# Kernel optimization log

Hardware: AMD Instinct MI355X
Metric: run time of the kernel (lower is better)

## Reference

```python
import jax, jax.numpy as jnp
import numpy as np

WIDTH = 256          # hidden width of FiLM MLP
NUM_FREQ = 8         # NeRF frequencies
BASE_FREQ = 1.25
TWO_PI = 2.0 * np.pi


def _uniform_linear(k, out_dim, in_dim):
    # torch nn.Linear default init: U(-1/sqrt(in), 1/sqrt(in))
    kw, kb = jax.random.split(k)
    s = 1.0 / np.sqrt(in_dim)
    W = jax.random.uniform(kw, (out_dim, in_dim), minval=-s, maxval=s, dtype=jnp.float32)
    b = jax.random.uniform(kb, (out_dim,), minval=-s, maxval=s, dtype=jnp.float32)
    return W, b


def setup_inputs() -> dict:
    key = jax.random.key(0)
    ks = jax.random.split(key, 14)
    B, T = 1024, 512
    latent_dim, lstm_hidden_dim = 128, 128
    spatial_dim, dir_dim, num_directions = 32, 8, 6
    emb_out = 2 * NUM_FREQ + 1                      # 17 (include_input)
    mod_in = latent_dim + lstm_hidden_dim + spatial_dim + dir_dim  # 296
    num_mods = 2 * WIDTH                            # width*(depth-1) = 512

    W_mod, b_mod = _uniform_linear(ks[0], num_mods, mod_in)
    W0, b0 = _uniform_linear(ks[1], WIDTH, emb_out)
    W1, b1 = _uniform_linear(ks[2], WIDTH, WIDTH)
    Wo, bo = _uniform_linear(ks[3], 1, WIDTH)
    Bmat = jax.random.normal(ks[4], (2, 16), dtype=jnp.float32) * 0.1  # sigma=0.1
    Ws1, bs1 = _uniform_linear(ks[5], 64, 32)
    Ws2, bs2 = _uniform_linear(ks[6], spatial_dim, 64)
    dir_emb = jax.random.normal(ks[7], (num_directions, dir_dim), dtype=jnp.float32)

    return dict(
        coords=jax.random.uniform(ks[8], (B, T, 1), dtype=jnp.float32),
        code=jax.random.normal(ks[9], (B, latent_dim), dtype=jnp.float32),
        hs=jax.random.normal(ks[10], (B, T, lstm_hidden_dim), dtype=jnp.float32),
        x_statics=jax.random.normal(ks[11], (B, 2), dtype=jnp.float32),
        dir_idx=jax.random.randint(ks[12], (1024,), 0, num_directions, dtype=jnp.int32),
        W_mod=W_mod, b_mod=b_mod, W0=W0, b0=b0, W1=W1, b1=b1, Wo=Wo, bo=bo,
        Bmat=Bmat, Ws1=Ws1, bs1=bs1, Ws2=Ws2, bs2=bs2, dir_emb=dir_emb,
    )


def reference(coords, code, hs, x_statics, dir_idx,
              W_mod, b_mod, W0, b0, W1, b1, Wo, bo,
              Bmat, Ws1, bs1, Ws2, bs2, dir_emb):
    B, T, _ = coords.shape

    # --- NeRF encoding: (B,T,1) -> (B,T,17) ---
    bands = BASE_FREQ * jnp.arange(0, NUM_FREQ, dtype=coords.dtype)     # (8,)
    winded = (coords[..., None, :] * bands[None, None, :, None]).reshape(B, T, -1)
    pos = jnp.concatenate([coords, jnp.sin(winded), jnp.cos(winded)], axis=-1)

    # --- Static encoder: latlon Fourier MLP + direction embedding ---
    proj = TWO_PI * (x_statics @ Bmat)                                  # (B,16)
    feats = jnp.concatenate([jnp.sin(proj), jnp.cos(proj)], axis=-1)    # (B,32)
    h = jax.nn.gelu(feats @ Ws1.T + bs1, approximate=False)             # (B,64)
    spatial = h @ Ws2.T + bs2                                           # (B,32)
    static_emb = jnp.concatenate([spatial, dir_emb[dir_idx]], axis=-1)  # (B,40)

    # --- Modulations: cat(code, h_t, static) -> 2*WIDTH, vectorized over T ---
    ctx = jnp.concatenate([
        jnp.broadcast_to(code[:, None, :], (B, T, code.shape[-1])),
        hs,
        jnp.broadcast_to(static_emb[:, None, :], (B, T, static_emb.shape[-1])),
    ], axis=-1)                                                         # (B,T,296)
    mods = jnp.einsum('btc,mc->btm', ctx, W_mod) + b_mod                # (B,T,512)

    # --- FiLM(shift)-modulated MLP: relu(Lin(x) + mod_chunk) per hidden layer ---
    x = jax.nn.relu(jnp.einsum('bte,we->btw', pos, W0) + b0 + mods[..., :WIDTH])
    x = jax.nn.relu(jnp.einsum('btw,vw->btv', x, W1) + b1 + mods[..., WIDTH:])
    out = jnp.einsum('btw,ow->bto', x, Wo) + bo                         # (B,T,1)
    return out
```

## Files before the change

kernel.cpp:

```cpp
#include <hip/hip_runtime.h>
#include <math.h>

typedef unsigned short ushort_t;
typedef __bf16 bf16x8 __attribute__((ext_vector_type(8)));
typedef __bf16 bf16x4 __attribute__((ext_vector_type(4)));
typedef float f32x4 __attribute__((ext_vector_type(4)));

#define TWO_PI_F 6.283185307179586f

#define WMT_OFF   0
#define PC_OFF    151552
#define WT0P_OFF  675840
#define WT1P_OFF  696320

__device__ __forceinline__ ushort_t f2bf(float f) {
  unsigned int u = __float_as_uint(f);
  u += 0x7fffu + ((u >> 16) & 1u);
  return (ushort_t)(u >> 16);
}

__global__ void pack_mfma_k(const float* __restrict__ W0,
                            const float* __restrict__ W1,
                            const float* __restrict__ W_mod,
                            float* __restrict__ WmT,
                            ushort_t* __restrict__ WT0p,
                            ushort_t* __restrict__ WT1p) {
  int i0 = blockIdx.x * blockDim.x + threadIdx.x;
  int stride = gridDim.x * blockDim.x;
  for (int idx = i0; idx < 296 * 512; idx += stride) {
    int c = idx >> 9, m = idx & 511;
    WmT[idx] = W_mod[m * 296 + c];
  }
  for (int e = i0; e < 40960; e += stride) {
    int j = e & 7, l = (e >> 3) & 63, nt = (e >> 9) & 15, ks = e >> 13;
    int k = ks * 32 + (l >> 4) * 8 + j;
    int n = nt * 16 + (l & 15);
    float v = 0.0f;
    if (k < 17) v = W0[n * 17 + k];
    else if (k >= 32) v = W_mod[n * 296 + 128 + (k - 32)];
    WT0p[e] = f2bf(v);
  }
  for (int e = i0; e < 98304; e += stride) {
    int j = e & 7, l = (e >> 3) & 63, nt = (e >> 9) & 15, ks = e >> 13;
    int k = ks * 32 + (l >> 4) * 8 + j;
    int n = nt * 16 + (l & 15);
    float v = (k < 256) ? W1[n * 256 + k]
                        : W_mod[(256 + n) * 296 + 128 + (k - 256)];
    WT1p[e] = f2bf(v);
  }
}

__global__ void precompute_pc_k(const float* __restrict__ code,
                                const float* __restrict__ x_statics,
                                const int* __restrict__ dir_idx,
                                const float* __restrict__ WmT,
                                const float* __restrict__ b_mod,
                                const float* __restrict__ b0,
                                const float* __restrict__ b1,
                                const float* __restrict__ Bmat,
                                const float* __restrict__ Ws1,
                                const float* __restrict__ bs1,
                                const float* __restrict__ Ws2,
                                const float* __restrict__ bs2,
                                const float* __restrict__ dir_emb,
                                float* __restrict__ pc) {
  int b = blockIdx.x, t = threadIdx.x;
  __shared__ float feats[32];
  __shared__ float h[64];
  __shared__ float se[40];
  __shared__ float cd[128];
  if (t < 16) {
    float p = TWO_PI_F * (x_statics[2 * b] * Bmat[t] + x_statics[2 * b + 1] * Bmat[16 + t]);
    feats[t] = sinf(p);
    feats[16 + t] = cosf(p);
  }
  if (t >= 128 && t < 256) cd[t - 128] = code[b * 128 + (t - 128)];
  __syncthreads();
  if (t < 64) {
    float a = bs1[t];
#pragma unroll
    for (int c = 0; c < 32; ++c) a = fmaf(feats[c], Ws1[t * 32 + c], a);
    h[t] = 0.5f * a * (1.0f + erff(a * 0.70710678118654752440f));
  }
  __syncthreads();
  if (t < 32) {
    float a = bs2[t];
#pragma unroll
    for (int c = 0; c < 64; ++c) a = fmaf(h[c], Ws2[t * 64 + c], a);
    se[t] = a;
  } else if (t < 40) {
    se[t] = dir_emb[dir_idx[b] * 8 + (t - 32)];
  }
  __syncthreads();
  float a = b_mod[t] + ((t < 256) ? b0[t] : b1[t - 256]);
  for (int c = 0; c < 128; ++c) a = fmaf(cd[c], WmT[c * 512 + t], a);
#pragma unroll
  for (int c = 0; c < 40; ++c) a = fmaf(se[c], WmT[(256 + c) * 512 + t], a);
  pc[b * 512 + t] = a;
}

__global__ __launch_bounds__(512, 2) void film_mfma(
    const float* __restrict__ coords, const float* __restrict__ hs,
    const float* __restrict__ pc, const ushort_t* __restrict__ WT0p,
    const ushort_t* __restrict__ WT1p, const float* __restrict__ Wo,
    const float* __restrict__ bo, float* __restrict__ out) {
  __shared__ uint4 rowbuf4[98304 / 16];
  __shared__ float pcs[512];
  __shared__ float psum[512];
  char* rowbuf = (char*)rowbuf4;

  const int tid = threadIdx.x;
  const int wv = tid >> 6;
  const int l = tid & 63;
  const int l4 = l & 15;
  const int hi4 = l >> 4;
  const int wr = wv >> 2;
  const int wc = wv & 3;
  const size_t row0 = (size_t)blockIdx.x * 128;
  const int b = blockIdx.x >> 2;

  pcs[tid] = pc[(size_t)b * 512 + tid];

  {
    const float4* hsv = (const float4*)(hs + row0 * 128);
#pragma unroll
    for (int it = 0; it < 8; ++it) {
      int idx = it * 512 + tid;
      int r = idx >> 5, c4 = idx & 31;
      float4 v = hsv[idx];
      bf16x4 hb;
      hb[0] = (__bf16)v.x; hb[1] = (__bf16)v.y;
      hb[2] = (__bf16)v.z; hb[3] = (__bf16)v.w;
      int byte = (r * 768 + 512 + c4 * 8) ^ ((r & 7) << 4);
      *(uint2*)(rowbuf + byte) = __builtin_bit_cast(uint2, hb);
    }
  }
  if (tid < 128) {
    int row = tid;
    float c = coords[row0 + row];
    __bf16 pv[32];
    pv[0] = (__bf16)c;
    pv[1] = (__bf16)0.0f;
    pv[9] = (__bf16)1.0f;
#pragma unroll
    for (int f = 1; f < 8; ++f) {
      float s, co;
      __sincosf(1.25f * (float)f * c, &s, &co);
      pv[1 + f] = (__bf16)s;
      pv[9 + f] = (__bf16)co;
    }
#pragma unroll
    for (int k = 17; k < 32; ++k) pv[k] = (__bf16)0.0f;
    int base = row * 768, swzp = (row & 7) << 4;
#pragma unroll
    for (int s = 0; s < 4; ++s)
      *(uint4*)(rowbuf + ((base + s * 16) ^ swzp)) = *(const uint4*)&pv[s * 8];
  }

  const int swz = (l4 & 7) << 4;
  int addrU[4];
#pragma unroll
  for (int mt = 0; mt < 4; ++mt)
    addrU[mt] = (wr * 64 + mt * 16 + l4) * 768 + hi4 * 16;

  __syncthreads();

  f32x4 acc[4][4];
#pragma unroll
  for (int mt = 0; mt < 4; ++mt)
#pragma unroll
    for (int i = 0; i < 4; ++i) acc[mt][i] = (f32x4){0.f, 0.f, 0.f, 0.f};

  {
    const uint4* Bb = (const uint4*)WT0p;
    bf16x8 wf[2][4];
#pragma unroll
    for (int i = 0; i < 4; ++i)
      wf[0][i] = __builtin_bit_cast(bf16x8, Bb[(1 * 16 + wc * 4 + i) * 64 + l]);
#pragma unroll
    for (int kk = 0; kk < 5; ++kk) {
      const int ks = (kk < 4) ? (kk + 1) : 0;
      const int cur = kk & 1;
      if (kk < 4) {
        const int ksn = (kk < 3) ? (kk + 2) : 0;
#pragma unroll
        for (int i = 0; i < 4; ++i)
          wf[cur ^ 1][i] = __builtin_bit_cast(bf16x8, Bb[(ksn * 16 + wc * 4 + i) * 64 + l]);
      }
#pragma unroll
      for (int mt = 0; mt < 4; ++mt) {
        bf16x8 u;
        int off = (ks == 0) ? addrU[mt] : (addrU[mt] + 512 + (ks - 1) * 64);
        __builtin_memcpy(&u, rowbuf + (off ^ swz), 16);
#pragma unroll
        for (int i = 0; i < 4; ++i)
          acc[mt][i] = __builtin_amdgcn_mfma_f32_16x16x32_bf16(wf[cur][i], u, acc[mt][i], 0, 0, 0);
      }
    }
  }
  __syncthreads();

#pragma unroll
  for (int i = 0; i < 4; ++i) {
    int n0 = wc * 64 + i * 16 + hi4 * 4;
    float4 p4 = *(const float4*)&pcs[n0];
#pragma unroll
    for (int mt = 0; mt < 4; ++mt) {
      int t = wr * 64 + mt * 16 + l4;
      bf16x4 hv;
      hv[0] = (__bf16)fmaxf(acc[mt][i][0] + p4.x, 0.f);
      hv[1] = (__bf16)fmaxf(acc[mt][i][1] + p4.y, 0.f);
      hv[2] = (__bf16)fmaxf(acc[mt][i][2] + p4.z, 0.f);
      hv[3] = (__bf16)fmaxf(acc[mt][i][3] + p4.w, 0.f);
      int byte = (t * 768 + n0 * 2) ^ ((t & 7) << 4);
      *(uint2*)(rowbuf + byte) = __builtin_bit_cast(uint2, hv);
    }
  }
  __syncthreads();

#pragma unroll
  for (int mt = 0; mt < 4; ++mt)
#pragma unroll
    for (int i = 0; i < 4; ++i) acc[mt][i] = (f32x4){0.f, 0.f, 0.f, 0.f};

  {
    const uint4* Bb = (const uint4*)WT1p;
    bf16x8 wf[2][4];
#pragma unroll
    for (int i = 0; i < 4; ++i)
      wf[0][i] = __builtin_bit_cast(bf16x8, Bb[(wc * 4 + i) * 64 + l]);
#pragma unroll
    for (int ks = 0; ks < 12; ++ks) {
      const int cur = ks & 1;
      if (ks < 11) {
#pragma unroll
        for (int i = 0; i < 4; ++i)
          wf[cur ^ 1][i] = __builtin_bit_cast(bf16x8, Bb[((ks + 1) * 16 + wc * 4 + i) * 64 + l]);
      }
#pragma unroll
      for (int mt = 0; mt < 4; ++mt) {
        bf16x8 u;
        __builtin_memcpy(&u, rowbuf + ((addrU[mt] + ks * 64) ^ swz), 16);
#pragma unroll
        for (int i = 0; i < 4; ++i)
          acc[mt][i] = __builtin_amdgcn_mfma_f32_16x16x32_bf16(wf[cur][i], u, acc[mt][i], 0, 0, 0);
      }
    }
  }

  {
    float4 p4[4], w4[4];
#pragma unroll
    for (int i = 0; i < 4; ++i) {
      int n0 = wc * 64 + i * 16 + hi4 * 4;
      p4[i] = *(const float4*)&pcs[256 + n0];
      w4[i] = ((const float4*)Wo)[(wc * 4 + i) * 4 + hi4];
    }
#pragma unroll
    for (int mt = 0; mt < 4; ++mt) {
      float s = 0.f;
#pragma unroll
      for (int i = 0; i < 4; ++i) {
        s += fmaxf(acc[mt][i][0] + p4[i].x, 0.f) * w4[i].x;
        s += fmaxf(acc[mt][i][1] + p4[i].y, 0.f) * w4[i].y;
        s += fmaxf(acc[mt][i][2] + p4[i].z, 0.f) * w4[i].z;
        s += fmaxf(acc[mt][i][3] + p4[i].w, 0.f) * w4[i].w;
      }
      s += __shfl_xor(s, 16);
      s += __shfl_xor(s, 32);
      if (hi4 == 0) psum[wc * 128 + wr * 64 + mt * 16 + l4] = s;
    }
  }
  __syncthreads();
  if (tid < 128) {
    float s = bo[0] + psum[tid] + psum[128 + tid] + psum[256 + tid] + psum[384 + tid];
    out[row0 + tid] = s;
  }
}

extern "C" void kernel_launch(void* const* d_in, const int* in_sizes, int n_in,
                              void* d_out, int out_size, void* d_ws, size_t ws_size,
                              hipStream_t stream) {
  (void)in_sizes; (void)n_in; (void)out_size; (void)ws_size;
  const float* coords    = (const float*)d_in[0];
  const float* code      = (const float*)d_in[1];
  const float* hs        = (const float*)d_in[2];
  const float* x_statics = (const float*)d_in[3];
  const int*   dir_idx   = (const int*)d_in[4];
  const float* W_mod     = (const float*)d_in[5];
  const float* b_mod     = (const float*)d_in[6];
  const float* W0        = (const float*)d_in[7];
  const float* b0        = (const float*)d_in[8];
  const float* W1        = (const float*)d_in[9];
  const float* b1        = (const float*)d_in[10];
  const float* Wo        = (const float*)d_in[11];
  const float* bo        = (const float*)d_in[12];
  const float* Bmat      = (const float*)d_in[13];
  const float* Ws1       = (const float*)d_in[14];
  const float* bs1       = (const float*)d_in[15];
  const float* Ws2       = (const float*)d_in[16];
  const float* bs2       = (const float*)d_in[17];
  const float* dir_emb   = (const float*)d_in[18];
  float* out = (float*)d_out;
  float* wsf = (float*)d_ws;

  float*    WmT  = wsf + WMT_OFF;
  float*    pc   = wsf + PC_OFF;
  ushort_t* WT0p = (ushort_t*)(wsf + WT0P_OFF);
  ushort_t* WT1p = (ushort_t*)(wsf + WT1P_OFF);

  hipLaunchKernelGGL(pack_mfma_k, dim3(1024), dim3(256), 0, stream,
                     W0, W1, W_mod, WmT, WT0p, WT1p);
  hipLaunchKernelGGL(precompute_pc_k, dim3(1024), dim3(512), 0, stream,
                     code, x_statics, dir_idx, WmT, b_mod, b0, b1,
                     Bmat, Ws1, bs1, Ws2, bs2, dir_emb, pc);
  hipLaunchKernelGGL(film_mfma, dim3(4096), dim3(512), 0, stream,
                     coords, hs, pc, WT0p, WT1p, Wo, bo, out);
}
```

Measured before the change: 193.1 us.

## Halve FiLM MLP block tile to 64 rows with 4 waves for higher occupancy

The main kernel now processes 64 rows per block with 256 threads (4 waves, each covering 64 output columns) instead of 128 rows with 8 waves, halving LDS per block so more blocks can be resident per CU. Weight fragments are prefetched as raw uint4 in registers, and the first layer-2 weight fetch is issued before the barrier. Smaller tiles mean each weight fragment loaded from global/L2 is reused across fewer rows, increasing weight traffic per output.

```diff
diff --git a/kernel.cpp b/kernel.cpp
--- a/kernel.cpp
+++ b/kernel.cpp
@@ -99,33 +99,32 @@
   pc[b * 512 + t] = a;
 }
 
-__global__ __launch_bounds__(512, 2) void film_mfma(
+__global__ __launch_bounds__(256, 3) void film_mfma(
     const float* __restrict__ coords, const float* __restrict__ hs,
     const float* __restrict__ pc, const ushort_t* __restrict__ WT0p,
     const ushort_t* __restrict__ WT1p, const float* __restrict__ Wo,
     const float* __restrict__ bo, float* __restrict__ out) {
-  __shared__ uint4 rowbuf4[98304 / 16];
+  __shared__ uint4 rowbuf4[49152 / 16];
   __shared__ float pcs[512];
-  __shared__ float psum[512];
+  __shared__ float psum[256];
   char* rowbuf = (char*)rowbuf4;
 
   const int tid = threadIdx.x;
-  const int wv = tid >> 6;
+  const int wc = tid >> 6;
   const int l = tid & 63;
   const int l4 = l & 15;
   const int hi4 = l >> 4;
-  const int wr = wv >> 2;
-  const int wc = wv & 3;
-  const size_t row0 = (size_t)blockIdx.x * 128;
-  const int b = blockIdx.x >> 2;
+  const size_t row0 = (size_t)blockIdx.x * 64;
+  const int b = blockIdx.x >> 3;
 
   pcs[tid] = pc[(size_t)b * 512 + tid];
+  pcs[tid + 256] = pc[(size_t)b * 512 + 256 + tid];
 
   {
     const float4* hsv = (const float4*)(hs + row0 * 128);
 #pragma unroll
     for (int it = 0; it < 8; ++it) {
-      int idx = it * 512 + tid;
+      int idx = it * 256 + tid;
       int r = idx >> 5, c4 = idx & 31;
       float4 v = hsv[idx];
       bf16x4 hb;
@@ -135,7 +134,7 @@
       *(uint2*)(rowbuf + byte) = __builtin_bit_cast(uint2, hb);
     }
   }
-  if (tid < 128) {
+  if (tid < 64) {
     int row = tid;
     float c = coords[row0 + row];
     __bf16 pv[32];
@@ -157,11 +156,18 @@
       *(uint4*)(rowbuf + ((base + s * 16) ^ swzp)) = *(const uint4*)&pv[s * 8];
   }
 
-  const int swz = (l4 & 7) << 4;
+  const int swzU = (l4 & 7) << 4;
   int addrU[4];
 #pragma unroll
   for (int mt = 0; mt < 4; ++mt)
-    addrU[mt] = (wr * 64 + mt * 16 + l4) * 768 + hi4 * 16;
+    addrU[mt] = (mt * 16 + l4) * 768 + hi4 * 16;
+
+  const uint4* Bb0 = (const uint4*)WT0p;
+  const uint4* Bb1 = (const uint4*)WT1p;
+
+  uint4 wp[4];
+#pragma unroll
+  for (int i = 0; i < 4; ++i) wp[i] = Bb0[(1 * 16 + wc * 4 + i) * 64 + l];
 
   __syncthreads();
 
@@ -171,42 +177,40 @@
 #pragma unroll
     for (int i = 0; i < 4; ++i) acc[mt][i] = (f32x4){0.f, 0.f, 0.f, 0.f};
 
-  {
-    const uint4* Bb = (const uint4*)WT0p;
-    bf16x8 wf[2][4];
-#pragma unroll
-    for (int i = 0; i < 4; ++i)
-      wf[0][i] = __builtin_bit_cast(bf16x8, Bb[(1 * 16 + wc * 4 + i) * 64 + l]);
-#pragma unroll
-    for (int kk = 0; kk < 5; ++kk) {
-      const int ks = (kk < 4) ? (kk + 1) : 0;
-      const int cur = kk & 1;
-      if (kk < 4) {
-        const int ksn = (kk < 3) ? (kk + 2) : 0;
-#pragma unroll
-        for (int i = 0; i < 4; ++i)
-          wf[cur ^ 1][i] = __builtin_bit_cast(bf16x8, Bb[(ksn * 16 + wc * 4 + i) * 64 + l]);
-      }
-#pragma unroll
-      for (int mt = 0; mt < 4; ++mt) {
-        bf16x8 u;
-        int off = (ks == 0) ? addrU[mt] : (addrU[mt] + 512 + (ks - 1) * 64);
-        __builtin_memcpy(&u, rowbuf + (off ^ swz), 16);
-#pragma unroll
-        for (int i = 0; i < 4; ++i)
-          acc[mt][i] = __builtin_amdgcn_mfma_f32_16x16x32_bf16(wf[cur][i], u, acc[mt][i], 0, 0, 0);
-      }
-    }
-  }
+#pragma unroll
+  for (int kk = 0; kk < 5; ++kk) {
+    const int ks = (kk < 4) ? (kk + 1) : 0;
+    bf16x8 w[4];
+#pragma unroll
+    for (int i = 0; i < 4; ++i) w[i] = __builtin_bit_cast(bf16x8, wp[i]);
+    if (kk < 4) {
+      const int ksn = (kk < 3) ? (kk + 2) : 0;
+#pragma unroll
+      for (int i = 0; i < 4; ++i) wp[i] = Bb0[(ksn * 16 + wc * 4 + i) * 64 + l];
+    }
+#pragma unroll
+    for (int mt = 0; mt < 4; ++mt) {
+      bf16x8 u;
+      int off = (ks == 0) ? addrU[mt] : (addrU[mt] + 512 + (ks - 1) * 64);
+      __builtin_memcpy(&u, rowbuf + (off ^ swzU), 16);
+#pragma unroll
+      for (int i = 0; i < 4; ++i)
+        acc[mt][i] = __builtin_amdgcn_mfma_f32_16x16x32_bf16(w[i], u, acc[mt][i], 0, 0, 0);
+    }
+  }
+
+#pragma unroll
+  for (int i = 0; i < 4; ++i) wp[i] = Bb1[(wc * 4 + i) * 64 + l];
+
   __syncthreads();
 
 #pragma unroll
   for (int i = 0; i < 4; ++i) {
-    int n0 = wc * 64 + i * 16 + hi4 * 4;
+    int n0 = (wc * 4 + i) * 16 + hi4 * 4;
     float4 p4 = *(const float4*)&pcs[n0];
 #pragma unroll
     for (int mt = 0; mt < 4; ++mt) {
-      int t = wr * 64 + mt * 16 + l4;
+      int t = mt * 16 + l4;
       bf16x4 hv;
       hv[0] = (__bf16)fmaxf(acc[mt][i][0] + p4.x, 0.f);
       hv[1] = (__bf16)fmaxf(acc[mt][i][1] + p4.y, 0.f);
@@ -223,28 +227,22 @@
 #pragma unroll
     for (int i = 0; i < 4; ++i) acc[mt][i] = (f32x4){0.f, 0.f, 0.f, 0.f};
 
-  {
-    const uint4* Bb = (const uint4*)WT1p;
-    bf16x8 wf[2][4];
-#pragma unroll
-    for (int i = 0; i < 4; ++i)
-      wf[0][i] = __builtin_bit_cast(bf16x8, Bb[(wc * 4 + i) * 64 + l]);
-#pragma unroll
-    for (int ks = 0; ks < 12; ++ks) {
-      const int cur = ks & 1;
-      if (ks < 11) {
-#pragma unroll
-        for (int i = 0; i < 4; ++i)
-          wf[cur ^ 1][i] = __builtin_bit_cast(bf16x8, Bb[((ks + 1) * 16 + wc * 4 + i) * 64 + l]);
-      }
-#pragma unroll
-      for (int mt = 0; mt < 4; ++mt) {
-        bf16x8 u;
-        __builtin_memcpy(&u, rowbuf + ((addrU[mt] + ks * 64) ^ swz), 16);
-#pragma unroll
-        for (int i = 0; i < 4; ++i)
-          acc[mt][i] = __builtin_amdgcn_mfma_f32_16x16x32_bf16(wf[cur][i], u, acc[mt][i], 0, 0, 0);
-      }
+#pragma unroll
+  for (int ks = 0; ks < 12; ++ks) {
+    bf16x8 w[4];
+#pragma unroll
+    for (int i = 0; i < 4; ++i) w[i] = __builtin_bit_cast(bf16x8, wp[i]);
+    if (ks < 11) {
+#pragma unroll
+      for (int i = 0; i < 4; ++i) wp[i] = Bb1[((ks + 1) * 16 + wc * 4 + i) * 64 + l];
+    }
+#pragma unroll
+    for (int mt = 0; mt < 4; ++mt) {
+      bf16x8 u;
+      __builtin_memcpy(&u, rowbuf + ((addrU[mt] + ks * 64) ^ swzU), 16);
+#pragma unroll
+      for (int i = 0; i < 4; ++i)
+        acc[mt][i] = __builtin_amdgcn_mfma_f32_16x16x32_bf16(w[i], u, acc[mt][i], 0, 0, 0);
     }
   }
 
@@ -252,7 +250,7 @@
     float4 p4[4], w4[4];
 #pragma unroll
     for (int i = 0; i < 4; ++i) {
-      int n0 = wc * 64 + i * 16 + hi4 * 4;
+      int n0 = (wc * 4 + i) * 16 + hi4 * 4;
       p4[i] = *(const float4*)&pcs[256 + n0];
       w4[i] = ((const float4*)Wo)[(wc * 4 + i) * 4 + hi4];
     }
@@ -268,12 +266,12 @@
       }
       s += __shfl_xor(s, 16);
       s += __shfl_xor(s, 32);
-      if (hi4 == 0) psum[wc * 128 + wr * 64 + mt * 16 + l4] = s;
-    }
-  }
-  __syncthreads();
-  if (tid < 128) {
-    float s = bo[0] + psum[tid] + psum[128 + tid] + psum[256 + tid] + psum[384 + tid];
+      if (hi4 == 0) psum[wc * 64 + mt * 16 + l4] = s;
+    }
+  }
+  __syncthreads();
+  if (tid < 64) {
+    float s = bo[0] + psum[tid] + psum[64 + tid] + psum[128 + tid] + psum[192 + tid];
     out[row0 + tid] = s;
   }
 }
@@ -314,6 +312,6 @@
   hipLaunchKernelGGL(precompute_pc_k, dim3(1024), dim3(512), 0, stream,
                      code, x_statics, dir_idx, WmT, b_mod, b0, b1,
                      Bmat, Ws1, bs1, Ws2, bs2, dir_emb, pc);
-  hipLaunchKernelGGL(film_mfma, dim3(4096), dim3(512), 0, stream,
+  hipLaunchKernelGGL(film_mfma, dim3(8192), dim3(256), 0, stream,
                      coords, hs, pc, WT0p, WT1p, Wo, bo, out);
 }
```

New measurement: 166.2 us. 13.9% less time.
